# Performance work log

Measured on AMD Instinct MI355X. Metric: run time of the kernel, lower is better.

The kernel has to match this reference:

```python
import jax, jax.numpy as jnp
from jax import lax
import numpy as np

L, D, HEADS, DH, FF = 12, 768, 12, 64, 3072
PATCH, IMG, B, S, OUT = 16, 224, 32, 197, 512


def setup_inputs() -> dict:
    key = jax.random.key(0)
    ks = jax.random.split(key, 10)
    nrm = lambda k, shp, s=0.02: jax.random.normal(k, shp, jnp.float32) * s
    return {
        "x_inp": jax.random.normal(ks[0], (B, 3, IMG, IMG), jnp.float32),
        "conv_w": nrm(ks[1], (D, 3, PATCH, PATCH)),
        "cls_emb": nrm(ks[2], (D,)),
        "pos_emb": nrm(ks[3], (S, D)),
        "ln_pre_w": jnp.ones((D,), jnp.float32),
        "ln_pre_b": jnp.zeros((D,), jnp.float32),
        "ln1_w": jnp.ones((L, D), jnp.float32),
        "ln1_b": jnp.zeros((L, D), jnp.float32),
        "qkv_w": nrm(ks[4], (L, 3 * D, D)),
        "qkv_b": jnp.zeros((L, 3 * D), jnp.float32),
        "out_w": nrm(ks[5], (L, D, D)),
        "out_b": jnp.zeros((L, D), jnp.float32),
        "ln2_w": jnp.ones((L, D), jnp.float32),
        "ln2_b": jnp.zeros((L, D), jnp.float32),
        "fc1_w": nrm(ks[6], (L, FF, D)),
        "fc1_b": jnp.zeros((L, FF), jnp.float32),
        "fc2_w": nrm(ks[7], (L, D, FF)),
        "fc2_b": jnp.zeros((L, D), jnp.float32),
        "ln_post_w": jnp.ones((D,), jnp.float32),
        "ln_post_b": jnp.zeros((D,), jnp.float32),
        "proj": nrm(ks[8], (D, OUT)),
    }


def _ln(x, w, b, eps=1e-5):
    mu = jnp.mean(x, axis=-1, keepdims=True)
    var = jnp.mean(jnp.square(x - mu), axis=-1, keepdims=True)
    return (x - mu) * lax.rsqrt(var + eps) * w + b


def _visual_forward(x_inp, conv_w, cls_emb, pos_emb, ln_pre_w, ln_pre_b,
                    ln1_w, ln1_b, qkv_w, qkv_b, out_w, out_b,
                    ln2_w, ln2_b, fc1_w, fc1_b, fc2_w, fc2_b,
                    ln_post_w, ln_post_b, proj):
    # patch embedding: conv stride=patch, no bias  -> [B, D, 14, 14]
    x = lax.conv_general_dilated(x_inp, conv_w, (PATCH, PATCH), 'VALID',
                                 dimension_numbers=('NCHW', 'OIHW', 'NCHW'))
    b = x.shape[0]
    x = x.reshape(b, D, -1).transpose(0, 2, 1)              # [B, 196, D]
    cls = jnp.broadcast_to(cls_emb, (b, 1, D))
    x = jnp.concatenate([cls, x], axis=1)                   # [B, 197, D]
    x = x + pos_emb[None]                                   # standard 197-token branch
    x = _ln(x, ln_pre_w, ln_pre_b)

    scale = float(DH) ** -0.5

    def block(h, p):
        l1w, l1b, qw, qb, ow, ob, l2w, l2b, f1w, f1b, f2w, f2b = p
        y = _ln(h, l1w, l1b)
        qkv = y @ qw.T + qb                                  # [B, S, 3D]
        q, k, v = jnp.split(qkv, 3, axis=-1)
        q = q.reshape(b, S, HEADS, DH) * scale
        k = k.reshape(b, S, HEADS, DH)
        v = v.reshape(b, S, HEADS, DH)
        attn = jnp.einsum('bqhd,bkhd->bhqk', q, k)
        attn = jax.nn.softmax(attn, axis=-1)
        o = jnp.einsum('bhqk,bkhd->bqhd', attn, v).reshape(b, S, D)
        h = h + o @ ow.T + ob
        y = _ln(h, l2w, l2b)
        y = y @ f1w.T + f1b
        y = y * jax.nn.sigmoid(1.702 * y)                    # QuickGELU
        h = h + y @ f2w.T + f2b
        return h, None

    params = (ln1_w, ln1_b, qkv_w, qkv_b, out_w, out_b,
              ln2_w, ln2_b, fc1_w, fc1_b, fc2_w, fc2_b)
    x, _ = lax.scan(block, x, params)

    cls_out = _ln(x[:, 0, :], ln_post_w, ln_post_b)
    return cls_out @ proj                                    # [B, 512]


def reference(x_inp, conv_w, cls_emb, pos_emb, ln_pre_w, ln_pre_b,
              ln1_w, ln1_b, qkv_w, qkv_b, out_w, out_b,
              ln2_w, ln2_b, fc1_w, fc1_b, fc2_w, fc2_b,
              ln_post_w, ln_post_b, proj):
    return _visual_forward(x_inp, conv_w, cls_emb, pos_emb, ln_pre_w, ln_pre_b,
                           ln1_w, ln1_b, qkv_w, qkv_b, out_w, out_b,
                           ln2_w, ln2_b, fc1_w, fc1_b, fc2_w, fc2_b,
                           ln_post_w, ln_post_b, proj)
```

## Files before the change

### kernel.cpp

```cpp
#include <hip/hip_runtime.h>
#include <hip/hip_bf16.h>


#define LAYERS 12
#define DMODEL 768
#define NHEADS 12
#define DHEAD  64
#define FFDIM  3072
#define BATCH  32
#define SEQ    197
#define NPATCH 196
#define OUTD   512
#define MROWS  (BATCH * SEQ)
#define MPAD   6400
#define SPAD   208
#define VSTR   208

typedef __attribute__((ext_vector_type(4))) float f32x4;
typedef __attribute__((ext_vector_type(8))) short bf16x8;

enum { M_F32 = 0, M_ACC = 1, M_GELU = 2, M_PATCH = 3, M_QKVB = 4 };

__device__ __forceinline__ float b2f(short s) {
    unsigned u = ((unsigned)(unsigned short)s) << 16;
    return __builtin_bit_cast(float, u);
}
__device__ __forceinline__ short f2b(float f) {
    __hip_bfloat16 h = __float2bfloat16(f);
    return __builtin_bit_cast(short, h);
}
__device__ __forceinline__ unsigned short f2bu(float f) {
    __hip_bfloat16 h = __float2bfloat16(f);
    return __builtin_bit_cast(unsigned short, h);
}

__device__ __forceinline__ void gl2lds16(const void* g, void* l) {
    __builtin_amdgcn_global_load_lds(
        (const __attribute__((address_space(1))) void*)g,
        (__attribute__((address_space(3))) void*)l, 16, 0, 0);
}

__global__ __launch_bounds__(256) void cvt_bf16_kernel(
    const float* __restrict__ src, __hip_bfloat16* __restrict__ dst, long n)
{
    long i0 = ((long)blockIdx.x * 256 + threadIdx.x) * 4;
    long stride = (long)gridDim.x * 1024;
    for (long i = i0; i < n; i += stride) {
        float4 v = *reinterpret_cast<const float4*>(&src[i]);
        ushort4 u;
        u.x = f2bu(v.x); u.y = f2bu(v.y); u.z = f2bu(v.z); u.w = f2bu(v.w);
        *reinterpret_cast<ushort4*>(&dst[i]) = u;
    }
}

__global__ __launch_bounds__(256) void im2col_kernel(
    const float* __restrict__ x_inp, __hip_bfloat16* __restrict__ patches)
{
    int bp = blockIdx.x;
    int b = bp / NPATCH, p = bp % NPATCH;
    int py = p / 14, px = p % 14;
    const float* xb = x_inp + (long)b * 3 * 224 * 224;
    for (int e = threadIdx.x; e < 768; e += 256) {
        int c = e >> 8, i = (e >> 4) & 15, j = e & 15;
        patches[(long)bp * 768 + e] =
            __float2bfloat16(xb[((long)c * 224 + py * 16 + i) * 224 + px * 16 + j]);
    }
}

__global__ __launch_bounds__(256) void cls_token_kernel(
    const float* __restrict__ cls_emb, const float* __restrict__ pos_emb,
    float* __restrict__ x)
{
    int b = blockIdx.x;
    for (int d = threadIdx.x; d < DMODEL; d += 256)
        x[(long)b * SEQ * DMODEL + d] = cls_emb[d] + pos_emb[d];
}

template<int OB>
__global__ __launch_bounds__(256) void ln_kernel(
    const float* __restrict__ in, void* __restrict__ out,
    const float* __restrict__ w, const float* __restrict__ bb,
    long in_stride, long out_stride, int nrows)
{
    int row = blockIdx.x * 4 + (threadIdx.x >> 6);
    if (row >= nrows) return;
    int lane = threadIdx.x & 63;
    const float* xr = in + (long)row * in_stride;

    float4 v[3];
    float s = 0.f;
    #pragma unroll
    for (int i = 0; i < 3; ++i) {
        v[i] = *reinterpret_cast<const float4*>(&xr[i * 256 + lane * 4]);
        s += v[i].x + v[i].y + v[i].z + v[i].w;
    }
    #pragma unroll
    for (int off = 32; off; off >>= 1) s += __shfl_xor(s, off);
    float mean = s * (1.0f / DMODEL);
    float sq = 0.f;
    #pragma unroll
    for (int i = 0; i < 3; ++i) {
        float a = v[i].x - mean, b2 = v[i].y - mean,
              c = v[i].z - mean, d = v[i].w - mean;
        sq += a * a + b2 * b2 + c * c + d * d;
    }
    #pragma unroll
    for (int off = 32; off; off >>= 1) sq += __shfl_xor(sq, off);
    float rstd = rsqrtf(sq * (1.0f / DMODEL) + 1e-5f);

    #pragma unroll
    for (int i = 0; i < 3; ++i) {
        int d0 = i * 256 + lane * 4;
        float4 wv = *reinterpret_cast<const float4*>(&w[d0]);
        float4 bv = *reinterpret_cast<const float4*>(&bb[d0]);
        float o0 = (v[i].x - mean) * rstd * wv.x + bv.x;
        float o1 = (v[i].y - mean) * rstd * wv.y + bv.y;
        float o2 = (v[i].z - mean) * rstd * wv.z + bv.z;
        float o3 = (v[i].w - mean) * rstd * wv.w + bv.w;
        if (OB) {
            ushort4 u;
            u.x = f2bu(o0); u.y = f2bu(o1); u.z = f2bu(o2); u.w = f2bu(o3);
            *reinterpret_cast<ushort4*>(
                &((__hip_bfloat16*)out)[(long)row * out_stride + d0]) = u;
        } else {
            float4 o = make_float4(o0, o1, o2, o3);
            *reinterpret_cast<float4*>(&((float*)out)[(long)row * out_stride + d0]) = o;
        }
    }
}

template<int MODE>
__global__ __launch_bounds__(256) void gemm_bf16(
    const __hip_bfloat16* __restrict__ A, const __hip_bfloat16* __restrict__ W,
    const float* __restrict__ bias, float* __restrict__ Cf,
    __hip_bfloat16* __restrict__ Cb, int M, int N, int K, int NB,
    const float* __restrict__ pos)
{
    __shared__ short As[2][64 * 64];
    __shared__ short Bs[2][128 * 64];
    int tid = threadIdx.x, lane = tid & 63, wv = tid >> 6;

    int nwg = gridDim.x, bid = blockIdx.x;
    int qq = nwg >> 3, rr = nwg & 7;
    int xcd = bid & 7, idx = bid >> 3;
    int newid = (xcd < rr ? xcd * (qq + 1) : rr * (qq + 1) + (xcd - rr) * qq) + idx;

    int bm = (newid / NB) * 64, bn = (newid % NB) * 128;
    int wn = wv * 32;
    f32x4 acc[4][2] = {};

    int sr = tid >> 3, sc = tid & 7;
    int c_log = sc ^ (sr & 7);
    const short* Ag = (const short*)A + (long)(bm + sr) * K + (c_log << 3);
    const short* Bg = (const short*)W + (long)(bn + sr) * K + (c_log << 3);
    const long K32 = (long)32 * K;

    int lg = lane >> 4, lr16 = lane & 15;
    int aoff[2][4], boff[2][2];
    #pragma unroll
    for (int s = 0; s < 2; ++s) {
        #pragma unroll
        for (int i = 0; i < 4; ++i) {
            int ra = i * 16 + lr16;
            aoff[s][i] = (ra << 6) + ((((s << 2) | lg) ^ (ra & 7)) << 3);
        }
        #pragma unroll
        for (int j = 0; j < 2; ++j) {
            int rb = wn + j * 16 + lr16;
            boff[s][j] = (rb << 6) + ((((s << 2) | lg) ^ (rb & 7)) << 3);
        }
    }

    const int KT = K >> 6;
    {
        char* Ad = (char*)&As[0][0]; char* Bd = (char*)&Bs[0][0];
        gl2lds16(Ag,           Ad + tid * 16);
        gl2lds16(Ag + K32,     Ad + 4096 + tid * 16);
        gl2lds16(Bg,           Bd + tid * 16);
        gl2lds16(Bg + K32,     Bd + 4096 + tid * 16);
        gl2lds16(Bg + 2 * K32, Bd + 8192 + tid * 16);
        gl2lds16(Bg + 3 * K32, Bd + 12288 + tid * 16);
    }
    __syncthreads();

    for (int t = 0; t < KT; ++t) {
        if (t + 1 < KT) {
            int ktn = (t + 1) << 6;
            char* Ad = (char*)&As[(t & 1) ^ 1][0];
            char* Bd = (char*)&Bs[(t & 1) ^ 1][0];
            gl2lds16(Ag + ktn,           Ad + tid * 16);
            gl2lds16(Ag + K32 + ktn,     Ad + 4096 + tid * 16);
            gl2lds16(Bg + ktn,           Bd + tid * 16);
            gl2lds16(Bg + K32 + ktn,     Bd + 4096 + tid * 16);
            gl2lds16(Bg + 2 * K32 + ktn, Bd + 8192 + tid * 16);
            gl2lds16(Bg + 3 * K32 + ktn, Bd + 12288 + tid * 16);
        }
        const short* Ab = &As[t & 1][0];
        const short* Bb = &Bs[t & 1][0];
        #pragma unroll
        for (int s = 0; s < 2; ++s) {
            bf16x8 af[4], bfr[2];
            #pragma unroll
            for (int i = 0; i < 4; ++i)
                af[i] = *reinterpret_cast<const bf16x8*>(&Ab[aoff[s][i]]);
            #pragma unroll
            for (int j = 0; j < 2; ++j)
                bfr[j] = *reinterpret_cast<const bf16x8*>(&Bb[boff[s][j]]);
            #pragma unroll
            for (int mi = 0; mi < 4; ++mi)
                #pragma unroll
                for (int ni = 0; ni < 2; ++ni)
                    acc[mi][ni] = __builtin_amdgcn_mfma_f32_16x16x32_bf16(
                        af[mi], bfr[ni], acc[mi][ni], 0, 0, 0);
        }
        __syncthreads();
    }

    #pragma unroll
    for (int mi = 0; mi < 4; ++mi) {
        int row0 = bm + mi * 16 + (lane >> 4) * 4;
        #pragma unroll
        for (int ni = 0; ni < 2; ++ni) {
            int col = bn + wn + ni * 16 + lr16;
            #pragma unroll
            for (int r = 0; r < 4; ++r) {
                int row = row0 + r;
                if (row >= M) continue;
                float v = acc[mi][ni][r];
                if (MODE == M_PATCH) {
                    int pb = row / 196, pp = row - pb * 196;
                    Cf[((long)(pb * SEQ + 1 + pp)) * DMODEL + col] =
                        v + pos[(long)(1 + pp) * DMODEL + col];
                } else {
                    v += bias[col];
                    long idx2 = (long)row * N + col;
                    if (MODE == M_F32)      Cf[idx2] = v;
                    else if (MODE == M_ACC) Cf[idx2] += v;
                    else if (MODE == M_QKVB) Cb[idx2] = __float2bfloat16(v);
                    else if (MODE == M_GELU)
                        Cb[idx2] = __float2bfloat16(v / (1.f + __expf(-1.702f * v)));
                }
            }
        }
    }
}

template<int MODE>
__global__ __launch_bounds__(256) void gemm128(
    const __hip_bfloat16* __restrict__ A, const __hip_bfloat16* __restrict__ W,
    const float* __restrict__ bias, __hip_bfloat16* __restrict__ Cb,
    int M, int N, int K, int NB)
{
    __shared__ short As[128 * 64];
    __shared__ short Bs[128 * 64];
    int tid = threadIdx.x, lane = tid & 63, wv = tid >> 6;

    int nwg = gridDim.x, bid = blockIdx.x;
    int qq = nwg >> 3, rr = nwg & 7;
    int xcd = bid & 7, idx = bid >> 3;
    int newid = (xcd < rr ? xcd * (qq + 1) : rr * (qq + 1) + (xcd - rr) * qq) + idx;

    int bm = (newid / NB) * 128, bn = (newid % NB) * 128;
    int wr = wv >> 1, wc = wv & 1;
    f32x4 acc[4][4] = {};

    int sr = tid >> 3, scn = tid & 7;
    int c_log = scn ^ (sr & 7);
    const short* Ag = (const short*)A + (long)(bm + sr) * K + (c_log << 3);
    const short* Bg = (const short*)W + (long)(bn + sr) * K + (c_log << 3);
    const long K32 = (long)32 * K;

    int lg = lane >> 4, lr16 = lane & 15;
    int aoff[2][4], boff[2][4];
    #pragma unroll
    for (int s = 0; s < 2; ++s) {
        int kc = (s << 2) | lg;
        #pragma unroll
        for (int i = 0; i < 4; ++i) {
            int ra = wr * 64 + i * 16 + lr16;
            aoff[s][i] = (ra << 6) + ((kc ^ (ra & 7)) << 3);
            int rb = wc * 64 + i * 16 + lr16;
            boff[s][i] = (rb << 6) + ((kc ^ (rb & 7)) << 3);
        }
    }

    const int KT = K >> 6;
    for (int t = 0; t < KT; ++t) {
        if (t) __syncthreads();
        int kt = t << 6;
        #pragma unroll
        for (int p = 0; p < 4; ++p) {
            gl2lds16(Ag + p * K32 + kt, (char*)As + p * 4096 + tid * 16);
            gl2lds16(Bg + p * K32 + kt, (char*)Bs + p * 4096 + tid * 16);
        }
        __syncthreads();

        #pragma unroll
        for (int s = 0; s < 2; ++s) {
            bf16x8 af[4], bfr[4];
            #pragma unroll
            for (int i = 0; i < 4; ++i)
                af[i] = *reinterpret_cast<const bf16x8*>(&As[aoff[s][i]]);
            #pragma unroll
            for (int j = 0; j < 4; ++j)
                bfr[j] = *reinterpret_cast<const bf16x8*>(&Bs[boff[s][j]]);
            #pragma unroll
            for (int mi = 0; mi < 4; ++mi)
                #pragma unroll
                for (int ni = 0; ni < 4; ++ni)
                    acc[mi][ni] = __builtin_amdgcn_mfma_f32_16x16x32_bf16(
                        af[mi], bfr[ni], acc[mi][ni], 0, 0, 0);
        }
    }

    #pragma unroll
    for (int mi = 0; mi < 4; ++mi) {
        int row0 = bm + wr * 64 + mi * 16 + lg * 4;
        #pragma unroll
        for (int ni = 0; ni < 4; ++ni) {
            int col = bn + wc * 64 + ni * 16 + lr16;
            #pragma unroll
            for (int r = 0; r < 4; ++r) {
                int row = row0 + r;
                if (row >= M) continue;
                float v = acc[mi][ni][r] + bias[col];
                long idx2 = (long)row * N + col;
                if (MODE == M_QKVB) Cb[idx2] = __float2bfloat16(v);
                else                Cb[idx2] = __float2bfloat16(v / (1.f + __expf(-1.702f * v)));
            }
        }
    }
}

__global__ __launch_bounds__(256) void attn_kernel(
    const __hip_bfloat16* __restrict__ qkv, __hip_bfloat16* __restrict__ o)
{
    int bh = blockIdx.x;
    int b = bh / NHEADS, h = bh % NHEADS;
    int tid = threadIdx.x, lane = tid & 63, wv = tid >> 6;
    __shared__ short Ks[SPAD * 64];
    __shared__ short Vt[64 * VSTR];
    __shared__ short Ps[4][16 * VSTR];
    const short* base = (const short*)qkv + (long)b * SEQ * 2304;

    for (int idx = tid; idx < SPAD * 8; idx += 256) {
        int r = idx >> 3, c = idx & 7;
        int4 val = make_int4(0, 0, 0, 0);
        if (r < SEQ)
            val = *reinterpret_cast<const int4*>(base + (long)r * 2304 + 768 + h * 64 + c * 8);
        *reinterpret_cast<int4*>(&Ks[r * 64 + ((c ^ (r & 7)) << 3)]) = val;
    }
    for (int idx = tid; idx < SPAD * 64; idx += 256) {
        int k = idx >> 6, d = idx & 63;
        short v = (k < SEQ) ? base[(long)k * 2304 + 1536 + h * 64 + d] : (short)0;
        Vt[d * VSTR + k] = v;
    }
    __syncthreads();

    int lg = lane >> 4, lr = lane & 15;
    short* Pw = Ps[wv];

    for (int ch = wv; ch < 13; ch += 4) {
        int q0 = ch * 16;
        const short* qp = (const short*)qkv +
            ((long)(b * SEQ) + q0 + lr) * 2304 + h * 64 + (lg << 3);
        bf16x8 qa = *reinterpret_cast<const bf16x8*>(qp);
        bf16x8 qb = *reinterpret_cast<const bf16x8*>(qp + 32);

        f32x4 sc[13];
        #pragma unroll
        for (int f = 0; f < 13; ++f) sc[f] = (f32x4){0.f, 0.f, 0.f, 0.f};
        #pragma unroll
        for (int f = 0; f < 13; ++f) {
            int row = f * 16 + lr;
            int sw = row & 7;
            const short* kr = &Ks[row * 64];
            bf16x8 k0 = *reinterpret_cast<const bf16x8*>(&kr[((lg + 0) ^ sw) << 3]);
            bf16x8 k1 = *reinterpret_cast<const bf16x8*>(&kr[((lg + 4) ^ sw) << 3]);
            sc[f] = __builtin_amdgcn_mfma_f32_16x16x32_bf16(qa, k0, sc[f], 0, 0, 0);
            sc[f] = __builtin_amdgcn_mfma_f32_16x16x32_bf16(qb, k1, sc[f], 0, 0, 0);
        }

        float mrow[4] = {-1e30f, -1e30f, -1e30f, -1e30f};
        #pragma unroll
        for (int f = 0; f < 13; ++f) {
            bool ok = f * 16 + lr < SEQ;
            #pragma unroll
            for (int r = 0; r < 4; ++r)
                if (ok) mrow[r] = fmaxf(mrow[r], sc[f][r] * 0.125f);
        }
        #pragma unroll
        for (int r = 0; r < 4; ++r)
            #pragma unroll
            for (int off = 8; off; off >>= 1)
                mrow[r] = fmaxf(mrow[r], __shfl_xor(mrow[r], off));
        float esum[4] = {0.f, 0.f, 0.f, 0.f};
        #pragma unroll
        for (int f = 0; f < 13; ++f) {
            bool ok = f * 16 + lr < SEQ;
            #pragma unroll
            for (int r = 0; r < 4; ++r) {
                float e = ok ? __expf(sc[f][r] * 0.125f - mrow[r]) : 0.f;
                sc[f][r] = e;
                esum[r] += e;
            }
        }
        #pragma unroll
        for (int r = 0; r < 4; ++r)
            #pragma unroll
            for (int off = 8; off; off >>= 1)
                esum[r] += __shfl_xor(esum[r], off);
        float inv[4];
        #pragma unroll
        for (int r = 0; r < 4; ++r) inv[r] = 1.0f / esum[r];

        #pragma unroll
        for (int f = 0; f < 13; ++f)
            #pragma unroll
            for (int r = 0; r < 4; ++r)
                Pw[(lg * 4 + r) * VSTR + f * 16 + lr] = f2b(sc[f][r] * inv[r]);

        f32x4 oa[4] = {};
        #pragma unroll
        for (int ks = 0; ks < 7; ++ks) {
            int kb = ks * 32 + (lg << 3);
            bf16x8 pa = {};
            if (kb < SPAD) pa = *reinterpret_cast<const bf16x8*>(&Pw[lr * VSTR + kb]);
            #pragma unroll
            for (int d = 0; d < 4; ++d) {
                bf16x8 vb = {};
                if (kb < SPAD)
                    vb = *reinterpret_cast<const bf16x8*>(&Vt[(d * 16 + lr) * VSTR + kb]);
                oa[d] = __builtin_amdgcn_mfma_f32_16x16x32_bf16(pa, vb, oa[d], 0, 0, 0);
            }
        }

        #pragma unroll
        for (int d = 0; d < 4; ++d)
            #pragma unroll
            for (int r = 0; r < 4; ++r) {
                int q = q0 + lg * 4 + r;
                if (q < SEQ)
                    o[((long)(b * SEQ + q)) * DMODEL + h * 64 + d * 16 + lr] =
                        __float2bfloat16(oa[d][r]);
            }
    }
}

__global__ __launch_bounds__(256) void proj_kernel(
    const float* __restrict__ cls_ln, const float* __restrict__ proj,
    float* __restrict__ out)
{
    int idx = blockIdx.x * 256 + threadIdx.x;
    int m = idx >> 9, n = idx & 511;
    float s = 0.f;
    #pragma unroll 8
    for (int k = 0; k < 768; ++k)
        s += cls_ln[m * 768 + k] * proj[k * 512 + n];
    out[idx] = s;
}

extern "C" void kernel_launch(void* const* d_in, const int* in_sizes, int n_in,
                              void* d_out, int out_size, void* d_ws, size_t ws_size,
                              hipStream_t stream) {
    const float* x_inp    = (const float*)d_in[0];
    const float* conv_w   = (const float*)d_in[1];
    const float* cls_emb  = (const float*)d_in[2];
    const float* pos_emb  = (const float*)d_in[3];
    const float* ln_pre_w = (const float*)d_in[4];
    const float* ln_pre_b = (const float*)d_in[5];
    const float* ln1_w    = (const float*)d_in[6];
    const float* ln1_b    = (const float*)d_in[7];
    const float* qkv_w    = (const float*)d_in[8];
    const float* qkv_b    = (const float*)d_in[9];
    const float* out_w    = (const float*)d_in[10];
    const float* out_b    = (const float*)d_in[11];
    const float* ln2_w    = (const float*)d_in[12];
    const float* ln2_b    = (const float*)d_in[13];
    const float* fc1_w    = (const float*)d_in[14];
    const float* fc1_b    = (const float*)d_in[15];
    const float* fc2_w    = (const float*)d_in[16];
    const float* fc2_b    = (const float*)d_in[17];
    const float* ln_post_w= (const float*)d_in[18];
    const float* ln_post_b= (const float*)d_in[19];
    const float* proj     = (const float*)d_in[20];

    char* w = (char*)d_ws;
    __hip_bfloat16* wqkv = (__hip_bfloat16*)w; w += (size_t)LAYERS * 2304 * DMODEL * 2;
    __hip_bfloat16* wout = (__hip_bfloat16*)w; w += (size_t)LAYERS * DMODEL * DMODEL * 2;
    __hip_bfloat16* wfc1 = (__hip_bfloat16*)w; w += (size_t)LAYERS * FFDIM * DMODEL * 2;
    __hip_bfloat16* wfc2 = (__hip_bfloat16*)w; w += (size_t)LAYERS * DMODEL * FFDIM * 2;
    __hip_bfloat16* wconv= (__hip_bfloat16*)w; w += (size_t)DMODEL * DMODEL * 2;
    float* x             = (float*)w;          w += (size_t)MROWS * DMODEL * 4;
    __hip_bfloat16* y    = (__hip_bfloat16*)w; w += (size_t)MPAD * DMODEL * 2;
    __hip_bfloat16* qkvb = (__hip_bfloat16*)w; w += (size_t)MPAD * 2304 * 2;
    __hip_bfloat16* attno= (__hip_bfloat16*)w; w += (size_t)MPAD * DMODEL * 2;
    __hip_bfloat16* h1   = (__hip_bfloat16*)w; w += (size_t)MPAD * FFDIM * 2;
    __hip_bfloat16* patches = (__hip_bfloat16*)w; w += (size_t)NPATCH * BATCH * DMODEL * 2;
    float* clsb          = (float*)w;          w += (size_t)BATCH * DMODEL * 4;

    cvt_bf16_kernel<<<2048, 256, 0, stream>>>(qkv_w, wqkv, (long)LAYERS * 2304 * DMODEL);
    cvt_bf16_kernel<<<2048, 256, 0, stream>>>(out_w, wout, (long)LAYERS * DMODEL * DMODEL);
    cvt_bf16_kernel<<<2048, 256, 0, stream>>>(fc1_w, wfc1, (long)LAYERS * FFDIM * DMODEL);
    cvt_bf16_kernel<<<2048, 256, 0, stream>>>(fc2_w, wfc2, (long)LAYERS * DMODEL * FFDIM);
    cvt_bf16_kernel<<<512, 256, 0, stream>>>(conv_w, wconv, (long)DMODEL * DMODEL);

    im2col_kernel<<<NPATCH * BATCH, 256, 0, stream>>>(x_inp, patches);
    gemm_bf16<M_PATCH><<<98 * 6, 256, 0, stream>>>(
        patches, wconv, nullptr, x, nullptr, NPATCH * BATCH, DMODEL, DMODEL, 6, pos_emb);
    cls_token_kernel<<<BATCH, 256, 0, stream>>>(cls_emb, pos_emb, x);
    ln_kernel<0><<<MROWS / 4, 256, 0, stream>>>(x, x, ln_pre_w, ln_pre_b,
                                                DMODEL, DMODEL, MROWS);

    for (int l = 0; l < LAYERS; ++l) {
        ln_kernel<1><<<MROWS / 4, 256, 0, stream>>>(x, y, ln1_w + l * DMODEL,
                                                    ln1_b + l * DMODEL, DMODEL, DMODEL, MROWS);
        gemm128<M_QKVB><<<50 * 18, 256, 0, stream>>>(
            y, wqkv + (long)l * 2304 * DMODEL, qkv_b + (long)l * 2304, qkvb,
            MROWS, 2304, DMODEL, 18);
        attn_kernel<<<BATCH * NHEADS, 256, 0, stream>>>(qkvb, attno);
        gemm_bf16<M_ACC><<<99 * 6, 256, 0, stream>>>(
            attno, wout + (long)l * DMODEL * DMODEL, out_b + (long)l * DMODEL, x, nullptr,
            MROWS, DMODEL, DMODEL, 6, nullptr);
        ln_kernel<1><<<MROWS / 4, 256, 0, stream>>>(x, y, ln2_w + l * DMODEL,
                                                    ln2_b + l * DMODEL, DMODEL, DMODEL, MROWS);
        gemm128<M_GELU><<<50 * 24, 256, 0, stream>>>(
            y, wfc1 + (long)l * FFDIM * DMODEL, fc1_b + (long)l * FFDIM, h1,
            MROWS, FFDIM, DMODEL, 24);
        gemm_bf16<M_ACC><<<99 * 6, 256, 0, stream>>>(
            h1, wfc2 + (long)l * DMODEL * FFDIM, fc2_b + (long)l * DMODEL, x, nullptr,
            MROWS, DMODEL, FFDIM, 6, nullptr);
    }

    ln_kernel<0><<<8, 256, 0, stream>>>(x, clsb, ln_post_w, ln_post_b,
                                        (long)SEQ * DMODEL, DMODEL, BATCH);
    proj_kernel<<<(BATCH * OUTD) / 256, 256, 0, stream>>>(clsb, proj, (float*)d_out);
}
```

Baseline: 3.173 ms.

## Switch 64x128 GEMM to single-buffered 128-deep K tiles

```diff
diff --git a/kernel.cpp b/kernel.cpp
--- a/kernel.cpp
+++ b/kernel.cpp
@@ -130,14 +130,14 @@
 }
 
 template<int MODE>
-__global__ __launch_bounds__(256) void gemm_bf16(
+__global__ __launch_bounds__(256) void gemm64k(
     const __hip_bfloat16* __restrict__ A, const __hip_bfloat16* __restrict__ W,
     const float* __restrict__ bias, float* __restrict__ Cf,
     __hip_bfloat16* __restrict__ Cb, int M, int N, int K, int NB,
     const float* __restrict__ pos)
 {
-    __shared__ short As[2][64 * 64];
-    __shared__ short Bs[2][128 * 64];
+    __shared__ short As[64 * 128];
+    __shared__ short Bs[128 * 128];
     int tid = threadIdx.x, lane = tid & 63, wv = tid >> 6;
 
     int nwg = gridDim.x, bid = blockIdx.x;
@@ -149,63 +149,50 @@
     int wn = wv * 32;
     f32x4 acc[4][2] = {};
 
-    int sr = tid >> 3, sc = tid & 7;
-    int c_log = sc ^ (sr & 7);
+    int sr = tid >> 4, scn = tid & 15;
+    int c_log = scn ^ sr;
     const short* Ag = (const short*)A + (long)(bm + sr) * K + (c_log << 3);
     const short* Bg = (const short*)W + (long)(bn + sr) * K + (c_log << 3);
-    const long K32 = (long)32 * K;
+    const long K16 = (long)16 * K;
 
     int lg = lane >> 4, lr16 = lane & 15;
-    int aoff[2][4], boff[2][2];
-    #pragma unroll
-    for (int s = 0; s < 2; ++s) {
+    int aoff[4][4], boff[4][2];
+    #pragma unroll
+    for (int s = 0; s < 4; ++s) {
+        int kc = (s << 2) | lg;
         #pragma unroll
         for (int i = 0; i < 4; ++i) {
             int ra = i * 16 + lr16;
-            aoff[s][i] = (ra << 6) + ((((s << 2) | lg) ^ (ra & 7)) << 3);
+            aoff[s][i] = (ra << 7) + (((kc ^ (ra & 15))) << 3);
         }
         #pragma unroll
         for (int j = 0; j < 2; ++j) {
             int rb = wn + j * 16 + lr16;
-            boff[s][j] = (rb << 6) + ((((s << 2) | lg) ^ (rb & 7)) << 3);
-        }
-    }
-
-    const int KT = K >> 6;
-    {
-        char* Ad = (char*)&As[0][0]; char* Bd = (char*)&Bs[0][0];
-        gl2lds16(Ag,           Ad + tid * 16);
-        gl2lds16(Ag + K32,     Ad + 4096 + tid * 16);
-        gl2lds16(Bg,           Bd + tid * 16);
-        gl2lds16(Bg + K32,     Bd + 4096 + tid * 16);
-        gl2lds16(Bg + 2 * K32, Bd + 8192 + tid * 16);
-        gl2lds16(Bg + 3 * K32, Bd + 12288 + tid * 16);
-    }
-    __syncthreads();
-
+            boff[s][j] = (rb << 7) + (((kc ^ (rb & 15))) << 3);
+        }
+    }
+
+    const int KT = K >> 7;
     for (int t = 0; t < KT; ++t) {
-        if (t + 1 < KT) {
-            int ktn = (t + 1) << 6;
-            char* Ad = (char*)&As[(t & 1) ^ 1][0];
-            char* Bd = (char*)&Bs[(t & 1) ^ 1][0];
-            gl2lds16(Ag + ktn,           Ad + tid * 16);
-            gl2lds16(Ag + K32 + ktn,     Ad + 4096 + tid * 16);
-            gl2lds16(Bg + ktn,           Bd + tid * 16);
-            gl2lds16(Bg + K32 + ktn,     Bd + 4096 + tid * 16);
-            gl2lds16(Bg + 2 * K32 + ktn, Bd + 8192 + tid * 16);
-            gl2lds16(Bg + 3 * K32 + ktn, Bd + 12288 + tid * 16);
-        }
-        const short* Ab = &As[t & 1][0];
-        const short* Bb = &Bs[t & 1][0];
-        #pragma unroll
-        for (int s = 0; s < 2; ++s) {
+        if (t) __syncthreads();
+        int kt = t << 7;
+        #pragma unroll
+        for (int p = 0; p < 4; ++p)
+            gl2lds16(Ag + p * K16 + kt, (char*)As + p * 4096 + tid * 16);
+        #pragma unroll
+        for (int p = 0; p < 8; ++p)
+            gl2lds16(Bg + p * K16 + kt, (char*)Bs + p * 4096 + tid * 16);
+        __syncthreads();
+
+        #pragma unroll
+        for (int s = 0; s < 4; ++s) {
             bf16x8 af[4], bfr[2];
             #pragma unroll
             for (int i = 0; i < 4; ++i)
-                af[i] = *reinterpret_cast<const bf16x8*>(&Ab[aoff[s][i]]);
+                af[i] = *reinterpret_cast<const bf16x8*>(&As[aoff[s][i]]);
             #pragma unroll
             for (int j = 0; j < 2; ++j)
-                bfr[j] = *reinterpret_cast<const bf16x8*>(&Bb[boff[s][j]]);
+                bfr[j] = *reinterpret_cast<const bf16x8*>(&Bs[boff[s][j]]);
             #pragma unroll
             for (int mi = 0; mi < 4; ++mi)
                 #pragma unroll
@@ -213,12 +200,11 @@
                     acc[mi][ni] = __builtin_amdgcn_mfma_f32_16x16x32_bf16(
                         af[mi], bfr[ni], acc[mi][ni], 0, 0, 0);
         }
-        __syncthreads();
     }
 
     #pragma unroll
     for (int mi = 0; mi < 4; ++mi) {
-        int row0 = bm + mi * 16 + (lane >> 4) * 4;
+        int row0 = bm + mi * 16 + lg * 4;
         #pragma unroll
         for (int ni = 0; ni < 2; ++ni) {
             int col = bn + wn + ni * 16 + lr16;
@@ -234,11 +220,8 @@
                 } else {
                     v += bias[col];
                     long idx2 = (long)row * N + col;
-                    if (MODE == M_F32)      Cf[idx2] = v;
-                    else if (MODE == M_ACC) Cf[idx2] += v;
-                    else if (MODE == M_QKVB) Cb[idx2] = __float2bfloat16(v);
-                    else if (MODE == M_GELU)
-                        Cb[idx2] = __float2bfloat16(v / (1.f + __expf(-1.702f * v)));
+                    if (MODE == M_ACC) Cf[idx2] += v;
+                    else               Cf[idx2] = v;
                 }
             }
         }
@@ -506,7 +489,7 @@
     cvt_bf16_kernel<<<512, 256, 0, stream>>>(conv_w, wconv, (long)DMODEL * DMODEL);
 
     im2col_kernel<<<NPATCH * BATCH, 256, 0, stream>>>(x_inp, patches);
-    gemm_bf16<M_PATCH><<<98 * 6, 256, 0, stream>>>(
+    gemm64k<M_PATCH><<<98 * 6, 256, 0, stream>>>(
         patches, wconv, nullptr, x, nullptr, NPATCH * BATCH, DMODEL, DMODEL, 6, pos_emb);
     cls_token_kernel<<<BATCH, 256, 0, stream>>>(cls_emb, pos_emb, x);
     ln_kernel<0><<<MROWS / 4, 256, 0, stream>>>(x, x, ln_pre_w, ln_pre_b,
@@ -519,7 +502,7 @@
             y, wqkv + (long)l * 2304 * DMODEL, qkv_b + (long)l * 2304, qkvb,
             MROWS, 2304, DMODEL, 18);
         attn_kernel<<<BATCH * NHEADS, 256, 0, stream>>>(qkvb, attno);
-        gemm_bf16<M_ACC><<<99 * 6, 256, 0, stream>>>(
+        gemm64k<M_ACC><<<99 * 6, 256, 0, stream>>>(
             attno, wout + (long)l * DMODEL * DMODEL, out_b + (long)l * DMODEL, x, nullptr,
             MROWS, DMODEL, DMODEL, 6, nullptr);
         ln_kernel<1><<<MROWS / 4, 256, 0, stream>>>(x, y, ln2_w + l * DMODEL,
@@ -527,7 +510,7 @@
         gemm128<M_GELU><<<50 * 24, 256, 0, stream>>>(
             y, wfc1 + (long)l * FFDIM * DMODEL, fc1_b + (long)l * FFDIM, h1,
             MROWS, FFDIM, DMODEL, 24);
-        gemm_bf16<M_ACC><<<99 * 6, 256, 0, stream>>>(
+        gemm64k<M_ACC><<<99 * 6, 256, 0, stream>>>(
             h1, wfc2 + (long)l * DMODEL * FFDIM, fc2_b + (long)l * DMODEL, x, nullptr,
             MROWS, DMODEL, FFDIM, 6, nullptr);
     }
```

Result: faster. 3.076 ms (-3.1%).
